# Kernel tuning notes

Hardware: AMD Instinct MI355X
Metric: run time of the kernel (lower is better)

The kernel has to match this reference:

```python
import jax, jax.numpy as jnp
import numpy as np

N_NODES = 50000
N_EDGES = 800000


def setup_inputs() -> dict:
    key = jax.random.key(0)
    ks = jax.random.split(key, 6)
    x = jax.random.normal(ks[0], (N_NODES, 22), dtype=jnp.float32)
    # small weight scale to keep tanh in its linear-ish regime
    W0 = jax.random.normal(ks[1], (22, 220), dtype=jnp.float32) * 0.1
    W1 = jax.random.normal(ks[2], (220, 220), dtype=jnp.float32) * 0.05
    W2 = jax.random.normal(ks[3], (220, 220), dtype=jnp.float32) * 0.05
    W3 = jax.random.normal(ks[4], (220, 10), dtype=jnp.float32) * 0.05
    b0 = jnp.zeros((220,), jnp.float32)
    b1 = jnp.zeros((220,), jnp.float32)
    b2 = jnp.zeros((220,), jnp.float32)
    b3 = jnp.zeros((10,), jnp.float32)
    edge_index = jax.random.randint(ks[5], (2, N_EDGES), 0, N_NODES, dtype=jnp.int64)
    return {"x": x, "W0": W0, "b0": b0, "W1": W1, "b1": b1,
            "W2": W2, "b2": b2, "W3": W3, "b3": b3, "edge_index": edge_index}


def _graph_conv(h, W, b, src, dst, inv_sqrt_out, inv_sqrt_in, activation):
    # DGL GraphConv, norm='both':
    #   h' = D_in^{-1/2} * A^T * (D_out^{-1/2} * h) @ W + b
    h = h * inv_sqrt_out[:, None]          # [N, F_in]
    m = h[src]                             # gather: [E, F_in]
    agg = jax.ops.segment_sum(m, dst, num_segments=N_NODES)  # scatter-add: [N, F_in]
    agg = agg * inv_sqrt_in[:, None]
    out = agg @ W + b
    if activation is not None:
        out = activation(out)
    return out


def reference(x, W0, b0, W1, b1, W2, b2, W3, b3, edge_index):
    src, dst = edge_index[0], edge_index[1]
    ones = jnp.ones((edge_index.shape[1],), jnp.float32)
    deg_out = jax.ops.segment_sum(ones, src, num_segments=N_NODES)
    deg_in = jax.ops.segment_sum(ones, dst, num_segments=N_NODES)
    inv_sqrt_out = jax.lax.rsqrt(jnp.maximum(deg_out, 1.0))
    inv_sqrt_in = jax.lax.rsqrt(jnp.maximum(deg_in, 1.0))

    h = _graph_conv(x, W0, b0, src, dst, inv_sqrt_out, inv_sqrt_in, jnp.tanh)
    h = _graph_conv(h, W1, b1, src, dst, inv_sqrt_out, inv_sqrt_in, jnp.tanh)
    h = _graph_conv(h, W2, b2, src, dst, inv_sqrt_out, inv_sqrt_in, jnp.tanh)
    h = _graph_conv(h, W3, b3, src, dst, inv_sqrt_out, inv_sqrt_in, None)
    return h
```

## Files before the change

kernel.cpp:

```cpp
#include <hip/hip_runtime.h>
#include <math.h>

#define N_NODES 50000
#define N_EDGES 800000
#define NPAD 50176
#define HSTR 224

typedef __attribute__((ext_vector_type(8))) short short8;
typedef __attribute__((ext_vector_type(4))) float f32x4;
typedef __attribute__((ext_vector_type(4))) _Float16 half4;


__device__ __forceinline__ float fast_tanh(float x) {
    float e = __expf(2.0f * x);
    float r = __builtin_amdgcn_rcpf(e + 1.0f);
    return 1.0f - 2.0f * r;
}

__device__ __forceinline__ unsigned short rne_bf16(float x) {
    unsigned u = __builtin_bit_cast(unsigned, x);
    return (unsigned short)((u + 0x7FFFu + ((u >> 16) & 1u)) >> 16);
}

__device__ __forceinline__ void split_bf16(float x, unsigned short& hi, unsigned short& lo) {
    hi = rne_bf16(x);
    float hf = __builtin_bit_cast(float, (unsigned)hi << 16);
    lo = rne_bf16(x - hf);
}

__device__ __forceinline__ f32x4 mfma16(short8 a, short8 b, f32x4 c) {
    return __builtin_amdgcn_mfma_f32_16x16x32_bf16(a, b, c, 0, 0, 0);
}

__device__ __forceinline__ void wsplit_one(const float* __restrict__ W, int KIN, int LDA,
                                           unsigned short* __restrict__ WT_hi,
                                           unsigned short* __restrict__ WT_lo, int idx) {
    int n = idx / LDA;
    int k = idx - n * LDA;
    float v = (n < 220 && k < KIN) ? W[k * 220 + n] : 0.f;
    unsigned short hi, lo;
    split_bf16(v, hi, lo);
    WT_hi[idx] = hi;
    WT_lo[idx] = lo;
}


__global__ void k_hist_wsplit(const int* __restrict__ ei, int* __restrict__ deg_out,
                              int* __restrict__ ecsbuf, int* __restrict__ rank,
                              const float* __restrict__ W0, const float* __restrict__ W1,
                              const float* __restrict__ W2,
                              unsigned short* __restrict__ wt0h, unsigned short* __restrict__ wt0l,
                              unsigned short* __restrict__ wt1h, unsigned short* __restrict__ wt1l,
                              unsigned short* __restrict__ wt2h, unsigned short* __restrict__ wt2l) {
    int bx = blockIdx.x;
    if (bx < 3125) {
        int e = bx * 256 + threadIdx.x;
        if (e < N_EDGES) {
            atomicAdd(&deg_out[ei[e]], 1);
            rank[e] = atomicAdd(&ecsbuf[1 + ei[N_EDGES + e]], 1);
        }
    } else if (bx < 3153) {
        int idx = (bx - 3125) * 256 + threadIdx.x;
        if (idx < 224 * 32) wsplit_one(W0, 22, 32, wt0h, wt0l, idx);
    } else if (bx < 3349) {
        int idx = (bx - 3153) * 256 + threadIdx.x;
        wsplit_one(W1, 220, 224, wt1h, wt1l, idx);
    } else {
        int idx = (bx - 3349) * 256 + threadIdx.x;
        wsplit_one(W2, 220, 224, wt2h, wt2l, idx);
    }
}

__global__ void k_scan1(const int* __restrict__ in, int* __restrict__ out,
                        int* __restrict__ bsum, int n) {
    __shared__ int s[256];
    int i = blockIdx.x * 256 + threadIdx.x;
    int v = (i < n) ? in[i] : 0;
    s[threadIdx.x] = v;
    __syncthreads();
    for (int off = 1; off < 256; off <<= 1) {
        int t = (threadIdx.x >= off) ? s[threadIdx.x - off] : 0;
        __syncthreads();
        s[threadIdx.x] += t;
        __syncthreads();
    }
    if (i < n) out[i] = s[threadIdx.x] - v;
    if (threadIdx.x == 255 && bsum) bsum[blockIdx.x] = s[255];
}

__global__ void k_scan_mid(int* __restrict__ a, int n) {
    __shared__ int s[256];
    __shared__ int carry;
    if (threadIdx.x == 0) carry = 0;
    for (int base = 0; base < n; base += 256) {
        int i = base + threadIdx.x;
        int v = (i < n) ? a[i] : 0;
        s[threadIdx.x] = v;
        __syncthreads();
        for (int off = 1; off < 256; off <<= 1) {
            int t = (threadIdx.x >= off) ? s[threadIdx.x - off] : 0;
            __syncthreads();
            s[threadIdx.x] += t;
            __syncthreads();
        }
        int c = carry;
        if (i < n) a[i] = s[threadIdx.x] - v + c;
        __syncthreads();
        if (threadIdx.x == 0) carry = c + s[255];
        __syncthreads();
    }
}

__global__ void k_scan3(int* __restrict__ out, const int* __restrict__ bscan, int n) {
    int i = blockIdx.x * 256 + threadIdx.x;
    if (i < n) out[i] += bscan[blockIdx.x];
}

__global__ void k_post_scan(const int* __restrict__ ei, const int* __restrict__ ecsbuf,
                            const int* __restrict__ rank, const int* __restrict__ deg_out,
                            const float* __restrict__ x,
                            float* __restrict__ inv_out, float* __restrict__ inv_in,
                            int* __restrict__ src_sorted, float* __restrict__ xs) {
    int bx = blockIdx.x;
    if (bx < 196) {
        int n = bx * 256 + threadIdx.x;
        if (n >= N_NODES) return;
        int di = ecsbuf[n + 2] - ecsbuf[n + 1];
        int a = deg_out[n]; if (a < 1) a = 1;
        if (di < 1) di = 1;
        inv_out[n] = 1.0f / sqrtf((float)a);
        inv_in[n]  = 1.0f / sqrtf((float)di);
    } else if (bx < 3321) {
        int e = (bx - 196) * 256 + threadIdx.x;
        if (e < N_EDGES) {
            int d = ei[N_EDGES + e];
            src_sorted[ecsbuf[1 + d] + rank[e]] = ei[e];
        }
    } else {
        int idx = (bx - 3321) * 256 + threadIdx.x;
        if (idx >= N_NODES * 11) return;
        int n = idx / 11;
        int f2 = idx - n * 11;
        int a = deg_out[n]; if (a < 1) a = 1;
        float sc = 1.0f / sqrtf((float)a);
        float2 v = *(const float2*)&x[n * 22 + f2 * 2];
        v.x *= sc; v.y *= sc;
        *(float2*)&xs[n * 22 + f2 * 2] = v;
    }
}


__global__ void k_agg22_split(const float* __restrict__ xs,
                              const int* __restrict__ ecsbuf, const int* __restrict__ srcs,
                              const float* __restrict__ inv_in,
                              unsigned short* __restrict__ A_hi, unsigned short* __restrict__ A_lo) {
    int idx = blockIdx.x * 256 + threadIdx.x;
    int n = idx >> 4, f2 = idx & 15;
    if (n >= N_NODES) return;
    float ax = 0.f, ay = 0.f;
    if (f2 <= 10) {
        const float2* xb = (const float2*)(xs) + f2;
        int e = ecsbuf[n + 1], end = ecsbuf[n + 2];
        for (; e + 3 < end; e += 4) {
            int s0 = srcs[e], s1 = srcs[e + 1], s2 = srcs[e + 2], s3 = srcs[e + 3];
            float2 v0 = xb[s0 * 11], v1 = xb[s1 * 11];
            float2 v2 = xb[s2 * 11], v3 = xb[s3 * 11];
            ax += (v0.x + v1.x) + (v2.x + v3.x);
            ay += (v0.y + v1.y) + (v2.y + v3.y);
        }
        for (; e < end; ++e) {
            float2 v0 = xb[srcs[e] * 11];
            ax += v0.x;
            ay += v0.y;
        }
        float si = inv_in[n];
        ax *= si; ay *= si;
    }
    ushort2 h2, l2;
    split_bf16(ax, h2.x, l2.x);
    split_bf16(ay, h2.y, l2.y);
    *(ushort2*)&A_hi[n * 32 + f2 * 2] = h2;
    *(ushort2*)&A_lo[n * 32 + f2 * 2] = l2;
}

__global__ __launch_bounds__(256) void k_agg220_split(const _Float16* __restrict__ h,
                                                      const int* __restrict__ ecsbuf,
                                                      const int* __restrict__ srcs,
                                                      const float* __restrict__ inv_in,
                                                      unsigned short* __restrict__ A_hi,
                                                      unsigned short* __restrict__ A_lo) {
    int lane = threadIdx.x & 63;
    int n = blockIdx.x * 4 + (threadIdx.x >> 6);
    if (n >= N_NODES || lane >= 56) return;
    size_t ob = (size_t)n * 224 + lane * 4;
    if (lane == 55) {
        ushort4 z = {0, 0, 0, 0};
        *(ushort4*)&A_hi[ob] = z;
        *(ushort4*)&A_lo[ob] = z;
        return;
    }
    int f4 = lane * 4;
    const _Float16* hb = h + f4;
    int e = ecsbuf[n + 1], end = ecsbuf[n + 2];
    float4 a0 = {0,0,0,0}, a1 = {0,0,0,0}, a2 = {0,0,0,0}, a3 = {0,0,0,0};
    for (; e + 7 < end; e += 8) {
        int s0 = srcs[e],     s1 = srcs[e + 1], s2 = srcs[e + 2], s3 = srcs[e + 3];
        int s4 = srcs[e + 4], s5 = srcs[e + 5], s6 = srcs[e + 6], s7 = srcs[e + 7];
        half4 v0 = *(const half4*)(hb + (size_t)s0 * HSTR);
        half4 v1 = *(const half4*)(hb + (size_t)s1 * HSTR);
        half4 v2 = *(const half4*)(hb + (size_t)s2 * HSTR);
        half4 v3 = *(const half4*)(hb + (size_t)s3 * HSTR);
        half4 v4 = *(const half4*)(hb + (size_t)s4 * HSTR);
        half4 v5 = *(const half4*)(hb + (size_t)s5 * HSTR);
        half4 v6 = *(const half4*)(hb + (size_t)s6 * HSTR);
        half4 v7 = *(const half4*)(hb + (size_t)s7 * HSTR);
        a0.x += (float)v0.x; a0.y += (float)v0.y; a0.z += (float)v0.z; a0.w += (float)v0.w;
        a1.x += (float)v1.x; a1.y += (float)v1.y; a1.z += (float)v1.z; a1.w += (float)v1.w;
        a2.x += (float)v2.x; a2.y += (float)v2.y; a2.z += (float)v2.z; a2.w += (float)v2.w;
        a3.x += (float)v3.x; a3.y += (float)v3.y; a3.z += (float)v3.z; a3.w += (float)v3.w;
        a0.x += (float)v4.x; a0.y += (float)v4.y; a0.z += (float)v4.z; a0.w += (float)v4.w;
        a1.x += (float)v5.x; a1.y += (float)v5.y; a1.z += (float)v5.z; a1.w += (float)v5.w;
        a2.x += (float)v6.x; a2.y += (float)v6.y; a2.z += (float)v6.z; a2.w += (float)v6.w;
        a3.x += (float)v7.x; a3.y += (float)v7.y; a3.z += (float)v7.z; a3.w += (float)v7.w;
    }
    for (; e + 3 < end; e += 4) {
        int s0 = srcs[e], s1 = srcs[e + 1], s2 = srcs[e + 2], s3 = srcs[e + 3];
        half4 v0 = *(const half4*)(hb + (size_t)s0 * HSTR);
        half4 v1 = *(const half4*)(hb + (size_t)s1 * HSTR);
        half4 v2 = *(const half4*)(hb + (size_t)s2 * HSTR);
        half4 v3 = *(const half4*)(hb + (size_t)s3 * HSTR);
        a0.x += (float)v0.x; a0.y += (float)v0.y; a0.z += (float)v0.z; a0.w += (float)v0.w;
        a1.x += (float)v1.x; a1.y += (float)v1.y; a1.z += (float)v1.z; a1.w += (float)v1.w;
        a2.x += (float)v2.x; a2.y += (float)v2.y; a2.z += (float)v2.z; a2.w += (float)v2.w;
        a3.x += (float)v3.x; a3.y += (float)v3.y; a3.z += (float)v3.z; a3.w += (float)v3.w;
    }
    for (; e < end; ++e) {
        half4 v = *(const half4*)(hb + (size_t)srcs[e] * HSTR);
        a0.x += (float)v.x; a0.y += (float)v.y; a0.z += (float)v.z; a0.w += (float)v.w;
    }
    float sc = inv_in[n];
    float4 t;
    t.x = ((a0.x + a1.x) + (a2.x + a3.x)) * sc;
    t.y = ((a0.y + a1.y) + (a2.y + a3.y)) * sc;
    t.z = ((a0.z + a1.z) + (a2.z + a3.z)) * sc;
    t.w = ((a0.w + a1.w) + (a2.w + a3.w)) * sc;
    ushort4 h4, l4;
    split_bf16(t.x, h4.x, l4.x);
    split_bf16(t.y, h4.y, l4.y);
    split_bf16(t.z, h4.z, l4.z);
    split_bf16(t.w, h4.w, l4.w);
    *(ushort4*)&A_hi[ob] = h4;
    *(ushort4*)&A_lo[ob] = l4;
}

__global__ void k_agg10_epi(const float* __restrict__ tmp, const int* __restrict__ ecsbuf,
                            const int* __restrict__ srcs, const float* __restrict__ inv_in,
                            const float* __restrict__ bias, float* __restrict__ out) {
    int idx = blockIdx.x * 256 + threadIdx.x;
    if (idx >= N_NODES * 5) return;
    int n = idx / 5;
    int f2 = idx - n * 5;
    const float2* tb0 = (const float2*)(tmp) + f2;
    const float2* tb1 = (const float2*)(tmp + (size_t)NPAD * 10) + f2;
    float ax = 0.f, ay = 0.f;
    int e = ecsbuf[n + 1], end = ecsbuf[n + 2];
    for (; e + 1 < end; e += 2) {
        float2 u0 = tb0[srcs[e] * 5],     w0 = tb1[srcs[e] * 5];
        float2 u1 = tb0[srcs[e + 1] * 5], w1 = tb1[srcs[e + 1] * 5];
        ax += (u0.x + w0.x) + (u1.x + w1.x);
        ay += (u0.y + w0.y) + (u1.y + w1.y);
    }
    if (e < end) {
        float2 u0 = tb0[srcs[e] * 5], w0 = tb1[srcs[e] * 5];
        ax += u0.x + w0.x;
        ay += u0.y + w0.y;
    }
    float si = inv_in[n];
    float2 o;
    o.x = ax * si + bias[f2 * 2];
    o.y = ay * si + bias[f2 * 2 + 1];
    *(float2*)&out[n * 10 + f2 * 2] = o;
}

template <int KSTEPS, int LDA, bool FUSE_W3>
__global__ __launch_bounds__(256, 4) void k_gemm_mfma(const unsigned short* __restrict__ A_hi,
                                                      const unsigned short* __restrict__ A_lo,
                                                      const unsigned short* __restrict__ WT_hi,
                                                      const unsigned short* __restrict__ WT_lo,
                                                      const float* __restrict__ bias,
                                                      const float* __restrict__ post,
                                                      _Float16* __restrict__ out,
                                                      const float* __restrict__ W3,
                                                      float* __restrict__ tmp) {
    int tid = threadIdx.x;
    int l = tid & 63, w = tid >> 6;
    int lrow = l & 15, q = l >> 4;
    int bid = blockIdx.x;
    int ch = bid & 1;
    int rt = (bid >> 1) * 64 + w * 16;
    int cb = ch * 112;

    const unsigned short* pah = A_hi + (size_t)(rt + lrow) * LDA + q * 8;
    const unsigned short* pal = A_lo + (size_t)(rt + lrow) * LDA + q * 8;
    const unsigned short* pbh = WT_hi + (size_t)(cb + lrow) * LDA + q * 8;
    const unsigned short* pbl = WT_lo + (size_t)(cb + lrow) * LDA + q * 8;

    f32x4 acc[7];
#pragma unroll
    for (int ct = 0; ct < 7; ++ct) acc[ct] = (f32x4){0.f, 0.f, 0.f, 0.f};

#pragma unroll
    for (int ks = 0; ks < KSTEPS; ++ks) {
        int k0 = ks * 32;
        short8 ah = *(const short8*)(const void*)(pah + k0);
        short8 al = *(const short8*)(const void*)(pal + k0);
#pragma unroll
        for (int ct = 0; ct < 7; ++ct) {
            size_t boff = (size_t)(ct * 16) * LDA + k0;
            short8 bh = *(const short8*)(const void*)(pbh + boff);
            short8 bl = *(const short8*)(const void*)(pbl + boff);
            acc[ct] = mfma16(ah, bh, acc[ct]);
            acc[ct] = mfma16(ah, bl, acc[ct]);
            acc[ct] = mfma16(al, bh, acc[ct]);
        }
    }

    float pv[4];
#pragma unroll
    for (int r = 0; r < 4; ++r) {
        int r0 = rt + q * 4 + r;
        pv[r] = (r0 < N_NODES) ? post[r0] : 0.f;
    }

    if (!FUSE_W3) {
#pragma unroll
        for (int ct = 0; ct < 7; ++ct) {
            int col = cb + ct * 16 + lrow;
            if (col >= 220) continue;
            float bv = bias[col];
#pragma unroll
            for (int r = 0; r < 4; ++r) {
                int r0 = rt + q * 4 + r;
                if (r0 < N_NODES)
                    out[(size_t)r0 * HSTR + col] = (_Float16)(pv[r] * fast_tanh(acc[ct][r] + bv));
            }
        }
    } else {
        float p[4][10];
#pragma unroll
        for (int r = 0; r < 4; ++r)
#pragma unroll
            for (int j = 0; j < 10; ++j) p[r][j] = 0.f;
#pragma unroll
        for (int ct = 0; ct < 7; ++ct) {
            int col = cb + ct * 16 + lrow;
            bool cok = col < 220;
            float bv = cok ? bias[col] : 0.f;
            float w3v[10];
            if (cok) {
                const float2* wp = (const float2*)&W3[col * 10];
#pragma unroll
                for (int j2 = 0; j2 < 5; ++j2) {
                    float2 t = wp[j2];
                    w3v[2 * j2] = t.x;
                    w3v[2 * j2 + 1] = t.y;
                }
            } else {
#pragma unroll
                for (int j = 0; j < 10; ++j) w3v[j] = 0.f;
            }
#pragma unroll
            for (int r = 0; r < 4; ++r) {
                float h2 = pv[r] * fast_tanh(acc[ct][r] + bv);
#pragma unroll
                for (int j = 0; j < 10; ++j) p[r][j] += h2 * w3v[j];
            }
        }
#pragma unroll
        for (int r = 0; r < 4; ++r)
#pragma unroll
            for (int j = 0; j < 10; ++j) {
                float v = p[r][j];
                v += __shfl_xor(v, 1, 64);
                v += __shfl_xor(v, 2, 64);
                v += __shfl_xor(v, 4, 64);
                v += __shfl_xor(v, 8, 64);
                p[r][j] = v;
            }
        if (lrow == 0) {
#pragma unroll
            for (int r = 0; r < 4; ++r) {
                int row = rt + q * 4 + r;
                if (row < N_NODES) {
                    float* tp = tmp + ((size_t)ch * NPAD + row) * 10;
#pragma unroll
                    for (int j2 = 0; j2 < 5; ++j2) {
                        float2 o = {p[r][2 * j2], p[r][2 * j2 + 1]};
                        *(float2*)&tp[2 * j2] = o;
                    }
                }
            }
        }
    }
}


extern "C" void kernel_launch(void* const* d_in, const int* in_sizes, int n_in,
                              void* d_out, int out_size, void* d_ws, size_t ws_size,
                              hipStream_t stream) {
    const float* x  = (const float*)d_in[0];
    const float* W0 = (const float*)d_in[1];
    const float* b0 = (const float*)d_in[2];
    const float* W1 = (const float*)d_in[3];
    const float* b1 = (const float*)d_in[4];
    const float* W2 = (const float*)d_in[5];
    const float* b2 = (const float*)d_in[6];
    const float* W3 = (const float*)d_in[7];
    const float* b3 = (const float*)d_in[8];
    const int*   ei = (const int*)d_in[9];
    float* out = (float*)d_out;

    int* ws = (int*)d_ws;
    int* ecsbuf     = ws + 0;
    int* deg_out    = ws + 50432;
    int* bsumA      = ws + 100608;
    float* inv_out  = (float*)(ws + 100864);
    float* inv_in   = (float*)(ws + 151040);
    int* src_sorted = ws + 201216;
    unsigned short* wt0h = (unsigned short*)(ws + 1001216);
    unsigned short* wt0l = (unsigned short*)(ws + 1004800);
    unsigned short* wt1h = (unsigned short*)(ws + 1008384);
    unsigned short* wt1l = (unsigned short*)(ws + 1033472);
    unsigned short* wt2h = (unsigned short*)(ws + 1058560);
    unsigned short* wt2l = (unsigned short*)(ws + 1083648);
    unsigned short* ahi  = (unsigned short*)(ws + 1108736);
    unsigned short* alo  = (unsigned short*)(ws + 6728448);
    _Float16* hbuf = (_Float16*)(ws + 12348160);
    float* tmp10 = (float*)(ws + 17948160);
    int* rank    = (int*)ahi;
    float* xs    = (float*)(ws + 1108736 + 3000000);

    hipMemsetAsync(ws, 0, (size_t)100608 * sizeof(int), stream);

    k_hist_wsplit<<<3545, 256, 0, stream>>>(ei, deg_out, ecsbuf, rank,
                                            W0, W1, W2, wt0h, wt0l, wt1h, wt1l, wt2h, wt2l);
    k_scan1<<<196, 256, 0, stream>>>(ecsbuf + 1, ecsbuf + 1, bsumA, NPAD);
    k_scan_mid<<<1, 256, 0, stream>>>(bsumA, 196);
    k_scan3<<<196, 256, 0, stream>>>(ecsbuf + 1, bsumA, NPAD);
    k_post_scan<<<5470, 256, 0, stream>>>(ei, ecsbuf, rank, deg_out, x,
                                          inv_out, inv_in, src_sorted, xs);

    int gemm_grid = (NPAD / 64) * 2;
    int agg_grid  = (N_NODES + 3) / 4;

    k_agg22_split<<<(N_NODES * 16 + 255) / 256, 256, 0, stream>>>(
        xs, ecsbuf, src_sorted, inv_in, ahi, alo);
    k_gemm_mfma<1, 32, false><<<gemm_grid, 256, 0, stream>>>(
        ahi, alo, wt0h, wt0l, b0, inv_out, hbuf, nullptr, nullptr);

    k_agg220_split<<<agg_grid, 256, 0, stream>>>(hbuf, ecsbuf, src_sorted, inv_in, ahi, alo);
    k_gemm_mfma<7, 224, false><<<gemm_grid, 256, 0, stream>>>(
        ahi, alo, wt1h, wt1l, b1, inv_out, hbuf, nullptr, nullptr);

    k_agg220_split<<<agg_grid, 256, 0, stream>>>(hbuf, ecsbuf, src_sorted, inv_in, ahi, alo);
    k_gemm_mfma<7, 224, true><<<gemm_grid, 256, 0, stream>>>(
        ahi, alo, wt2h, wt2l, b2, inv_out, nullptr, W3, tmp10);

    k_agg10_epi<<<(N_NODES * 5 + 255) / 256, 256, 0, stream>>>(
        tmp10, ecsbuf, src_sorted, inv_in, b3, out);
}
```

Baseline: 465.8 us.

## Double rows per warp in MFMA GEMM and batch histogram edges per thread

Each warp in the split-bf16 MFMA GEMM now computes two 16-row tiles instead of one, so every B (weight) fragment loaded is reused across twice as many rows. Block row coverage goes from 64 to 128 and the grid is halved. The launch-bounds occupancy hint drops from 4 to 3 to make room for the doubled accumulators. Separately, the histogram kernel has each thread handle four edges, cutting its block count; the cost is higher register pressure and fewer waves for latency hiding.

Result: no change. 473.8 us (+1.7%).

```diff
diff --git a/kernel.cpp b/kernel.cpp
--- a/kernel.cpp
+++ b/kernel.cpp
@@ -53,20 +53,24 @@
                               unsigned short* __restrict__ wt1h, unsigned short* __restrict__ wt1l,
                               unsigned short* __restrict__ wt2h, unsigned short* __restrict__ wt2l) {
     int bx = blockIdx.x;
-    if (bx < 3125) {
-        int e = bx * 256 + threadIdx.x;
-        if (e < N_EDGES) {
-            atomicAdd(&deg_out[ei[e]], 1);
-            rank[e] = atomicAdd(&ecsbuf[1 + ei[N_EDGES + e]], 1);
-        }
-    } else if (bx < 3153) {
-        int idx = (bx - 3125) * 256 + threadIdx.x;
+    if (bx < 782) {
+        int base = bx * 1024 + threadIdx.x;
+#pragma unroll
+        for (int i = 0; i < 4; ++i) {
+            int e = base + i * 256;
+            if (e < N_EDGES) {
+                atomicAdd(&deg_out[ei[e]], 1);
+                rank[e] = atomicAdd(&ecsbuf[1 + ei[N_EDGES + e]], 1);
+            }
+        }
+    } else if (bx < 810) {
+        int idx = (bx - 782) * 256 + threadIdx.x;
         if (idx < 224 * 32) wsplit_one(W0, 22, 32, wt0h, wt0l, idx);
-    } else if (bx < 3349) {
-        int idx = (bx - 3153) * 256 + threadIdx.x;
+    } else if (bx < 1006) {
+        int idx = (bx - 810) * 256 + threadIdx.x;
         wsplit_one(W1, 220, 224, wt1h, wt1l, idx);
     } else {
-        int idx = (bx - 3349) * 256 + threadIdx.x;
+        int idx = (bx - 1006) * 256 + threadIdx.x;
         wsplit_one(W2, 220, 224, wt2h, wt2l, idx);
     }
 }
@@ -283,7 +287,7 @@
 }
 
 template <int KSTEPS, int LDA, bool FUSE_W3>
-__global__ __launch_bounds__(256, 4) void k_gemm_mfma(const unsigned short* __restrict__ A_hi,
+__global__ __launch_bounds__(256, 3) void k_gemm_mfma(const unsigned short* __restrict__ A_hi,
                                                       const unsigned short* __restrict__ A_lo,
                                                       const unsigned short* __restrict__ WT_hi,
                                                       const unsigned short* __restrict__ WT_lo,
@@ -297,39 +301,51 @@
     int lrow = l & 15, q = l >> 4;
     int bid = blockIdx.x;
     int ch = bid & 1;
-    int rt = (bid >> 1) * 64 + w * 16;
+    int rt = (bid >> 1) * 128 + w * 32;
     int cb = ch * 112;
 
-    const unsigned short* pah = A_hi + (size_t)(rt + lrow) * LDA + q * 8;
-    const unsigned short* pal = A_lo + (size_t)(rt + lrow) * LDA + q * 8;
+    const unsigned short* pa0h = A_hi + (size_t)(rt + lrow) * LDA + q * 8;
+    const unsigned short* pa0l = A_lo + (size_t)(rt + lrow) * LDA + q * 8;
+    const unsigned short* pa1h = pa0h + 16 * LDA;
+    const unsigned short* pa1l = pa0l + 16 * LDA;
     const unsigned short* pbh = WT_hi + (size_t)(cb + lrow) * LDA + q * 8;
     const unsigned short* pbl = WT_lo + (size_t)(cb + lrow) * LDA + q * 8;
 
-    f32x4 acc[7];
-#pragma unroll
-    for (int ct = 0; ct < 7; ++ct) acc[ct] = (f32x4){0.f, 0.f, 0.f, 0.f};
+    f32x4 acc0[7], acc1[7];
+#pragma unroll
+    for (int ct = 0; ct < 7; ++ct) {
+        acc0[ct] = (f32x4){0.f, 0.f, 0.f, 0.f};
+        acc1[ct] = (f32x4){0.f, 0.f, 0.f, 0.f};
+    }
 
 #pragma unroll
     for (int ks = 0; ks < KSTEPS; ++ks) {
         int k0 = ks * 32;
-        short8 ah = *(const short8*)(const void*)(pah + k0);
-        short8 al = *(const short8*)(const void*)(pal + k0);
+        short8 ah0 = *(const short8*)(const void*)(pa0h + k0);
+        short8 al0 = *(const short8*)(const void*)(pa0l + k0);
+        short8 ah1 = *(const short8*)(const void*)(pa1h + k0);
+        short8 al1 = *(const short8*)(const void*)(pa1l + k0);
 #pragma unroll
         for (int ct = 0; ct < 7; ++ct) {
             size_t boff = (size_t)(ct * 16) * LDA + k0;
             short8 bh = *(const short8*)(const void*)(pbh + boff);
             short8 bl = *(const short8*)(const void*)(pbl + boff);
-            acc[ct] = mfma16(ah, bh, acc[ct]);
-            acc[ct] = mfma16(ah, bl, acc[ct]);
-            acc[ct] = mfma16(al, bh, acc[ct]);
-        }
-    }
-
-    float pv[4];
+            acc0[ct] = mfma16(ah0, bh, acc0[ct]);
+            acc0[ct] = mfma16(ah0, bl, acc0[ct]);
+            acc0[ct] = mfma16(al0, bh, acc0[ct]);
+            acc1[ct] = mfma16(ah1, bh, acc1[ct]);
+            acc1[ct] = mfma16(ah1, bl, acc1[ct]);
+            acc1[ct] = mfma16(al1, bh, acc1[ct]);
+        }
+    }
+
+    float pv0[4], pv1[4];
 #pragma unroll
     for (int r = 0; r < 4; ++r) {
         int r0 = rt + q * 4 + r;
-        pv[r] = (r0 < N_NODES) ? post[r0] : 0.f;
+        int r1 = r0 + 16;
+        pv0[r] = (r0 < N_NODES) ? post[r0] : 0.f;
+        pv1[r] = (r1 < N_NODES) ? post[r1] : 0.f;
     }
 
     if (!FUSE_W3) {
@@ -341,62 +357,71 @@
 #pragma unroll
             for (int r = 0; r < 4; ++r) {
                 int r0 = rt + q * 4 + r;
+                int r1 = r0 + 16;
                 if (r0 < N_NODES)
-                    out[(size_t)r0 * HSTR + col] = (_Float16)(pv[r] * fast_tanh(acc[ct][r] + bv));
+                    out[(size_t)r0 * HSTR + col] = (_Float16)(pv0[r] * fast_tanh(acc0[ct][r] + bv));
+                if (r1 < N_NODES)
+                    out[(size_t)r1 * HSTR + col] = (_Float16)(pv1[r] * fast_tanh(acc1[ct][r] + bv));
             }
         }
     } else {
-        float p[4][10];
-#pragma unroll
-        for (int r = 0; r < 4; ++r)
-#pragma unroll
-            for (int j = 0; j < 10; ++j) p[r][j] = 0.f;
-#pragma unroll
-        for (int ct = 0; ct < 7; ++ct) {
-            int col = cb + ct * 16 + lrow;
-            bool cok = col < 220;
-            float bv = cok ? bias[col] : 0.f;
-            float w3v[10];
-            if (cok) {
-                const float2* wp = (const float2*)&W3[col * 10];
-#pragma unroll
-                for (int j2 = 0; j2 < 5; ++j2) {
-                    float2 t = wp[j2];
-                    w3v[2 * j2] = t.x;
-                    w3v[2 * j2 + 1] = t.y;
+#pragma unroll
+        for (int half = 0; half < 2; ++half) {
+            const f32x4* acc = half ? acc1 : acc0;
+            const float* pv  = half ? pv1 : pv0;
+            int rbase = rt + half * 16;
+            float p[4][10];
+#pragma unroll
+            for (int r = 0; r < 4; ++r)
+#pragma unroll
+                for (int j = 0; j < 10; ++j) p[r][j] = 0.f;
+#pragma unroll
+            for (int ct = 0; ct < 7; ++ct) {
+                int col = cb + ct * 16 + lrow;
+                bool cok = col < 220;
+                float bv = cok ? bias[col] : 0.f;
+                float w3v[10];
+                if (cok) {
+                    const float2* wp = (const float2*)&W3[col * 10];
+#pragma unroll
+                    for (int j2 = 0; j2 < 5; ++j2) {
+                        float2 t = wp[j2];
+                        w3v[2 * j2] = t.x;
+                        w3v[2 * j2 + 1] = t.y;
+                    }
+                } else {
+#pragma unroll
+                    for (int j = 0; j < 10; ++j) w3v[j] = 0.f;
                 }
-            } else {
-#pragma unroll
-                for (int j = 0; j < 10; ++j) w3v[j] = 0.f;
+#pragma unroll
+                for (int r = 0; r < 4; ++r) {
+                    float h2 = pv[r] * fast_tanh(acc[ct][r] + bv);
+#pragma unroll
+                    for (int j = 0; j < 10; ++j) p[r][j] += h2 * w3v[j];
+                }
             }
 #pragma unroll
-            for (int r = 0; r < 4; ++r) {
-                float h2 = pv[r] * fast_tanh(acc[ct][r] + bv);
-#pragma unroll
-                for (int j = 0; j < 10; ++j) p[r][j] += h2 * w3v[j];
-            }
-        }
-#pragma unroll
-        for (int r = 0; r < 4; ++r)
-#pragma unroll
-            for (int j = 0; j < 10; ++j) {
-                float v = p[r][j];
-                v += __shfl_xor(v, 1, 64);
-                v += __shfl_xor(v, 2, 64);
-                v += __shfl_xor(v, 4, 64);
-                v += __shfl_xor(v, 8, 64);
-                p[r][j] = v;
-            }
-        if (lrow == 0) {
-#pragma unroll
-            for (int r = 0; r < 4; ++r) {
-                int row = rt + q * 4 + r;
-                if (row < N_NODES) {
-                    float* tp = tmp + ((size_t)ch * NPAD + row) * 10;
-#pragma unroll
-                    for (int j2 = 0; j2 < 5; ++j2) {
-                        float2 o = {p[r][2 * j2], p[r][2 * j2 + 1]};
-                        *(float2*)&tp[2 * j2] = o;
+            for (int r = 0; r < 4; ++r)
+#pragma unroll
+                for (int j = 0; j < 10; ++j) {
+                    float v = p[r][j];
+                    v += __shfl_xor(v, 1, 64);
+                    v += __shfl_xor(v, 2, 64);
+                    v += __shfl_xor(v, 4, 64);
+                    v += __shfl_xor(v, 8, 64);
+                    p[r][j] = v;
+                }
+            if (lrow == 0) {
+#pragma unroll
+                for (int r = 0; r < 4; ++r) {
+                    int row = rbase + q * 4 + r;
+                    if (row < N_NODES) {
+                        float* tp = tmp + ((size_t)ch * NPAD + row) * 10;
+#pragma unroll
+                        for (int j2 = 0; j2 < 5; ++j2) {
+                            float2 o = {p[r][2 * j2], p[r][2 * j2 + 1]};
+                            *(float2*)&tp[2 * j2] = o;
+                        }
                     }
                 }
             }
@@ -442,7 +467,7 @@
 
     hipMemsetAsync(ws, 0, (size_t)100608 * sizeof(int), stream);
 
-    k_hist_wsplit<<<3545, 256, 0, stream>>>(ei, deg_out, ecsbuf, rank,
+    k_hist_wsplit<<<1202, 256, 0, stream>>>(ei, deg_out, ecsbuf, rank,
                                             W0, W1, W2, wt0h, wt0l, wt1h, wt1l, wt2h, wt2l);
     k_scan1<<<196, 256, 0, stream>>>(ecsbuf + 1, ecsbuf + 1, bsumA, NPAD);
     k_scan_mid<<<1, 256, 0, stream>>>(bsumA, 196);
@@ -450,7 +475,7 @@
     k_post_scan<<<5470, 256, 0, stream>>>(ei, ecsbuf, rank, deg_out, x,
                                           inv_out, inv_in, src_sorted, xs);
 
-    int gemm_grid = (NPAD / 64) * 2;
+    int gemm_grid = (NPAD / 128) * 2;
     int agg_grid  = (N_NODES + 3) / 4;
 
     k_agg22_split<<<(N_NODES * 16 + 255) / 256, 256, 0, stream>>>(
```

## Compute full 224 columns per GEMM block and drop partial-sum split in layer 3

Applied to the files above, without the earlier changes.

The MFMA GEMM now has each wave compute all 14 column tiles instead of splitting columns across two blocks. This halves the grid and removes the redundant A-fragment reloads. In the W3-fused layer, the two half-column partial outputs and their summation in the final aggregation are no longer needed, so k_agg10_epi gathers one buffer instead of two. The histogram kernel also processes four edges per thread with fewer blocks. The cost is twice as many accumulator registers under launch_bounds(256,4), which risks spills or lower occupancy, and half as many blocks to spread across the GPU.

Result: slower. 577.9 us (+24.1%).

```diff
diff --git a/kernel.cpp b/kernel.cpp
--- a/kernel.cpp
+++ b/kernel.cpp
@@ -53,20 +53,24 @@
                               unsigned short* __restrict__ wt1h, unsigned short* __restrict__ wt1l,
                               unsigned short* __restrict__ wt2h, unsigned short* __restrict__ wt2l) {
     int bx = blockIdx.x;
-    if (bx < 3125) {
-        int e = bx * 256 + threadIdx.x;
-        if (e < N_EDGES) {
-            atomicAdd(&deg_out[ei[e]], 1);
-            rank[e] = atomicAdd(&ecsbuf[1 + ei[N_EDGES + e]], 1);
-        }
-    } else if (bx < 3153) {
-        int idx = (bx - 3125) * 256 + threadIdx.x;
+    if (bx < 782) {
+        int base = bx * 1024 + threadIdx.x;
+#pragma unroll
+        for (int i = 0; i < 4; ++i) {
+            int e = base + i * 256;
+            if (e < N_EDGES) {
+                atomicAdd(&deg_out[ei[e]], 1);
+                rank[e] = atomicAdd(&ecsbuf[1 + ei[N_EDGES + e]], 1);
+            }
+        }
+    } else if (bx < 810) {
+        int idx = (bx - 782) * 256 + threadIdx.x;
         if (idx < 224 * 32) wsplit_one(W0, 22, 32, wt0h, wt0l, idx);
-    } else if (bx < 3349) {
-        int idx = (bx - 3153) * 256 + threadIdx.x;
+    } else if (bx < 1006) {
+        int idx = (bx - 810) * 256 + threadIdx.x;
         wsplit_one(W1, 220, 224, wt1h, wt1l, idx);
     } else {
-        int idx = (bx - 3349) * 256 + threadIdx.x;
+        int idx = (bx - 1006) * 256 + threadIdx.x;
         wsplit_one(W2, 220, 224, wt2h, wt2l, idx);
     }
 }
@@ -260,20 +264,19 @@
     if (idx >= N_NODES * 5) return;
     int n = idx / 5;
     int f2 = idx - n * 5;
-    const float2* tb0 = (const float2*)(tmp) + f2;
-    const float2* tb1 = (const float2*)(tmp + (size_t)NPAD * 10) + f2;
+    const float2* tb = (const float2*)(tmp) + f2;
     float ax = 0.f, ay = 0.f;
     int e = ecsbuf[n + 1], end = ecsbuf[n + 2];
     for (; e + 1 < end; e += 2) {
-        float2 u0 = tb0[srcs[e] * 5],     w0 = tb1[srcs[e] * 5];
-        float2 u1 = tb0[srcs[e + 1] * 5], w1 = tb1[srcs[e + 1] * 5];
-        ax += (u0.x + w0.x) + (u1.x + w1.x);
-        ay += (u0.y + w0.y) + (u1.y + w1.y);
+        float2 v0 = tb[srcs[e] * 5];
+        float2 v1 = tb[srcs[e + 1] * 5];
+        ax += v0.x + v1.x;
+        ay += v0.y + v1.y;
     }
     if (e < end) {
-        float2 u0 = tb0[srcs[e] * 5], w0 = tb1[srcs[e] * 5];
-        ax += u0.x + w0.x;
-        ay += u0.y + w0.y;
+        float2 v0 = tb[srcs[e] * 5];
+        ax += v0.x;
+        ay += v0.y;
     }
     float si = inv_in[n];
     float2 o;
@@ -295,19 +298,16 @@
     int tid = threadIdx.x;
     int l = tid & 63, w = tid >> 6;
     int lrow = l & 15, q = l >> 4;
-    int bid = blockIdx.x;
-    int ch = bid & 1;
-    int rt = (bid >> 1) * 64 + w * 16;
-    int cb = ch * 112;
+    int rt = blockIdx.x * 64 + w * 16;
 
     const unsigned short* pah = A_hi + (size_t)(rt + lrow) * LDA + q * 8;
     const unsigned short* pal = A_lo + (size_t)(rt + lrow) * LDA + q * 8;
-    const unsigned short* pbh = WT_hi + (size_t)(cb + lrow) * LDA + q * 8;
-    const unsigned short* pbl = WT_lo + (size_t)(cb + lrow) * LDA + q * 8;
-
-    f32x4 acc[7];
-#pragma unroll
-    for (int ct = 0; ct < 7; ++ct) acc[ct] = (f32x4){0.f, 0.f, 0.f, 0.f};
+    const unsigned short* pbh = WT_hi + (size_t)lrow * LDA + q * 8;
+    const unsigned short* pbl = WT_lo + (size_t)lrow * LDA + q * 8;
+
+    f32x4 acc[14];
+#pragma unroll
+    for (int ct = 0; ct < 14; ++ct) acc[ct] = (f32x4){0.f, 0.f, 0.f, 0.f};
 
 #pragma unroll
     for (int ks = 0; ks < KSTEPS; ++ks) {
@@ -315,7 +315,7 @@
         short8 ah = *(const short8*)(const void*)(pah + k0);
         short8 al = *(const short8*)(const void*)(pal + k0);
 #pragma unroll
-        for (int ct = 0; ct < 7; ++ct) {
+        for (int ct = 0; ct < 14; ++ct) {
             size_t boff = (size_t)(ct * 16) * LDA + k0;
             short8 bh = *(const short8*)(const void*)(pbh + boff);
             short8 bl = *(const short8*)(const void*)(pbl + boff);
@@ -334,8 +334,8 @@
 
     if (!FUSE_W3) {
 #pragma unroll
-        for (int ct = 0; ct < 7; ++ct) {
-            int col = cb + ct * 16 + lrow;
+        for (int ct = 0; ct < 14; ++ct) {
+            int col = ct * 16 + lrow;
             if (col >= 220) continue;
             float bv = bias[col];
 #pragma unroll
@@ -346,57 +346,60 @@
             }
         }
     } else {
-        float p[4][10];
-#pragma unroll
-        for (int r = 0; r < 4; ++r)
-#pragma unroll
-            for (int j = 0; j < 10; ++j) p[r][j] = 0.f;
-#pragma unroll
-        for (int ct = 0; ct < 7; ++ct) {
-            int col = cb + ct * 16 + lrow;
-            bool cok = col < 220;
-            float bv = cok ? bias[col] : 0.f;
-            float w3v[10];
-            if (cok) {
-                const float2* wp = (const float2*)&W3[col * 10];
-#pragma unroll
-                for (int j2 = 0; j2 < 5; ++j2) {
-                    float2 t = wp[j2];
-                    w3v[2 * j2] = t.x;
-                    w3v[2 * j2 + 1] = t.y;
+#pragma unroll
+        for (int rc = 0; rc < 2; ++rc) {
+            float p[2][10];
+#pragma unroll
+            for (int r2 = 0; r2 < 2; ++r2)
+#pragma unroll
+                for (int j = 0; j < 10; ++j) p[r2][j] = 0.f;
+#pragma unroll
+            for (int ct = 0; ct < 14; ++ct) {
+                int col = ct * 16 + lrow;
+                bool cok = col < 220;
+                float bv = cok ? bias[col] : 0.f;
+                float w3v[10];
+                if (cok) {
+                    const float2* wp = (const float2*)&W3[col * 10];
+#pragma unroll
+                    for (int j2 = 0; j2 < 5; ++j2) {
+                        float2 t = wp[j2];
+                        w3v[2 * j2] = t.x;
+                        w3v[2 * j2 + 1] = t.y;
+                    }
+                } else {
+#pragma unroll
+                    for (int j = 0; j < 10; ++j) w3v[j] = 0.f;
                 }
-            } else {
-#pragma unroll
-                for (int j = 0; j < 10; ++j) w3v[j] = 0.f;
+#pragma unroll
+                for (int r2 = 0; r2 < 2; ++r2) {
+                    int r = rc * 2 + r2;
+                    float h2 = pv[r] * fast_tanh(acc[ct][r] + bv);
+#pragma unroll
+                    for (int j = 0; j < 10; ++j) p[r2][j] += h2 * w3v[j];
+                }
             }
 #pragma unroll
-            for (int r = 0; r < 4; ++r) {
-                float h2 = pv[r] * fast_tanh(acc[ct][r] + bv);
-#pragma unroll
-                for (int j = 0; j < 10; ++j) p[r][j] += h2 * w3v[j];
-            }
-        }
-#pragma unroll
-        for (int r = 0; r < 4; ++r)
-#pragma unroll
-            for (int j = 0; j < 10; ++j) {
-                float v = p[r][j];
-                v += __shfl_xor(v, 1, 64);
-                v += __shfl_xor(v, 2, 64);
-                v += __shfl_xor(v, 4, 64);
-                v += __shfl_xor(v, 8, 64);
-                p[r][j] = v;
-            }
-        if (lrow == 0) {
-#pragma unroll
-            for (int r = 0; r < 4; ++r) {
-                int row = rt + q * 4 + r;
-                if (row < N_NODES) {
-                    float* tp = tmp + ((size_t)ch * NPAD + row) * 10;
-#pragma unroll
-                    for (int j2 = 0; j2 < 5; ++j2) {
-                        float2 o = {p[r][2 * j2], p[r][2 * j2 + 1]};
-                        *(float2*)&tp[2 * j2] = o;
+            for (int r2 = 0; r2 < 2; ++r2)
+#pragma unroll
+                for (int j = 0; j < 10; ++j) {
+                    float v = p[r2][j];
+                    v += __shfl_xor(v, 1, 64);
+                    v += __shfl_xor(v, 2, 64);
+                    v += __shfl_xor(v, 4, 64);
+                    v += __shfl_xor(v, 8, 64);
+                    p[r2][j] = v;
+                }
+            if (lrow == 0) {
+#pragma unroll
+                for (int r2 = 0; r2 < 2; ++r2) {
+                    int row = rt + q * 4 + rc * 2 + r2;
+                    if (row < N_NODES) {
+#pragma unroll
+                        for (int j2 = 0; j2 < 5; ++j2) {
+                            float2 o = {p[r2][2 * j2], p[r2][2 * j2 + 1]};
+                            *(float2*)&tmp[(size_t)row * 10 + 2 * j2] = o;
+                        }
                     }
                 }
             }
@@ -442,7 +445,7 @@
 
     hipMemsetAsync(ws, 0, (size_t)100608 * sizeof(int), stream);
 
-    k_hist_wsplit<<<3545, 256, 0, stream>>>(ei, deg_out, ecsbuf, rank,
+    k_hist_wsplit<<<1202, 256, 0, stream>>>(ei, deg_out, ecsbuf, rank,
                                             W0, W1, W2, wt0h, wt0l, wt1h, wt1l, wt2h, wt2l);
     k_scan1<<<196, 256, 0, stream>>>(ecsbuf + 1, ecsbuf + 1, bsumA, NPAD);
     k_scan_mid<<<1, 256, 0, stream>>>(bsumA, 196);
@@ -450,7 +453,7 @@
     k_post_scan<<<5470, 256, 0, stream>>>(ei, ecsbuf, rank, deg_out, x,
                                           inv_out, inv_in, src_sorted, xs);
 
-    int gemm_grid = (NPAD / 64) * 2;
+    int gemm_grid = NPAD / 64;
     int agg_grid  = (N_NODES + 3) / 4;
 
     k_agg22_split<<<(N_NODES * 16 + 255) / 256, 256, 0, stream>>>(
```

## Privatize degree histograms into eight copies to cut atomic contention

Applied to the files above, without the earlier changes.

The degree/count histogram is split into eight private copies chosen by block index, each block now handles four edges per thread, and the rank is packed together with the copy id. A new k_sum8 kernel reduces the copies into per-copy prefix offsets and totals, and the scatter into sorted order adds the per-copy prefix. This is meant to spread same-address atomics over eight locations. In exchange it adds a kernel launch and a larger memset, and the pass keeps its existing cost on 800K edges.

After: 466.2 us. About the same (+0.1%).

```diff
diff --git a/kernel.cpp b/kernel.cpp
--- a/kernel.cpp
+++ b/kernel.cpp
@@ -45,30 +45,57 @@
 }
 
 
-__global__ void k_hist_wsplit(const int* __restrict__ ei, int* __restrict__ deg_out,
-                              int* __restrict__ ecsbuf, int* __restrict__ rank,
+__global__ void k_hist_wsplit(const int* __restrict__ ei, int* __restrict__ deg8,
+                              int* __restrict__ cnt8, int* __restrict__ rank,
                               const float* __restrict__ W0, const float* __restrict__ W1,
                               const float* __restrict__ W2,
                               unsigned short* __restrict__ wt0h, unsigned short* __restrict__ wt0l,
                               unsigned short* __restrict__ wt1h, unsigned short* __restrict__ wt1l,
                               unsigned short* __restrict__ wt2h, unsigned short* __restrict__ wt2l) {
     int bx = blockIdx.x;
-    if (bx < 3125) {
-        int e = bx * 256 + threadIdx.x;
-        if (e < N_EDGES) {
-            atomicAdd(&deg_out[ei[e]], 1);
-            rank[e] = atomicAdd(&ecsbuf[1 + ei[N_EDGES + e]], 1);
-        }
-    } else if (bx < 3153) {
-        int idx = (bx - 3125) * 256 + threadIdx.x;
+    if (bx < 782) {
+        int c = bx & 7;
+        int* degc = deg8 + c * NPAD;
+        int* cntc = cnt8 + c * NPAD;
+        int base = bx * 1024 + threadIdx.x;
+#pragma unroll
+        for (int i = 0; i < 4; ++i) {
+            int e = base + i * 256;
+            if (e < N_EDGES) {
+                atomicAdd(&degc[ei[e]], 1);
+                int r = atomicAdd(&cntc[ei[N_EDGES + e]], 1);
+                rank[e] = (r << 3) | c;
+            }
+        }
+    } else if (bx < 810) {
+        int idx = (bx - 782) * 256 + threadIdx.x;
         if (idx < 224 * 32) wsplit_one(W0, 22, 32, wt0h, wt0l, idx);
-    } else if (bx < 3349) {
-        int idx = (bx - 3153) * 256 + threadIdx.x;
+    } else if (bx < 1006) {
+        int idx = (bx - 810) * 256 + threadIdx.x;
         wsplit_one(W1, 220, 224, wt1h, wt1l, idx);
     } else {
-        int idx = (bx - 3349) * 256 + threadIdx.x;
+        int idx = (bx - 1006) * 256 + threadIdx.x;
         wsplit_one(W2, 220, 224, wt2h, wt2l, idx);
     }
+}
+
+__global__ void k_sum8(int* __restrict__ cnt8, const int* __restrict__ deg8,
+                       int* __restrict__ ecsbuf, int* __restrict__ deg_out) {
+    int d = blockIdx.x * 256 + threadIdx.x;
+    if (d >= NPAD) return;
+    int s = 0;
+#pragma unroll
+    for (int c = 0; c < 8; ++c) {
+        int v = cnt8[c * NPAD + d];
+        cnt8[c * NPAD + d] = s;
+        s += v;
+    }
+    ecsbuf[1 + d] = s;
+    if (d == 0) ecsbuf[0] = 0;
+    int t = 0;
+#pragma unroll
+    for (int c = 0; c < 8; ++c) t += deg8[c * NPAD + d];
+    deg_out[d] = t;
 }
 
 __global__ void k_scan1(const int* __restrict__ in, int* __restrict__ out,
@@ -117,8 +144,8 @@
 }
 
 __global__ void k_post_scan(const int* __restrict__ ei, const int* __restrict__ ecsbuf,
-                            const int* __restrict__ rank, const int* __restrict__ deg_out,
-                            const float* __restrict__ x,
+                            const int* __restrict__ rank, const int* __restrict__ prefix8,
+                            const int* __restrict__ deg_out, const float* __restrict__ x,
                             float* __restrict__ inv_out, float* __restrict__ inv_in,
                             int* __restrict__ src_sorted, float* __restrict__ xs) {
     int bx = blockIdx.x;
@@ -134,7 +161,9 @@
         int e = (bx - 196) * 256 + threadIdx.x;
         if (e < N_EDGES) {
             int d = ei[N_EDGES + e];
-            src_sorted[ecsbuf[1 + d] + rank[e]] = ei[e];
+            int rc = rank[e];
+            int c = rc & 7, r = rc >> 3;
+            src_sorted[ecsbuf[1 + d] + prefix8[c * NPAD + d] + r] = ei[e];
         }
     } else {
         int idx = (bx - 3321) * 256 + threadIdx.x;
@@ -437,17 +466,20 @@
     unsigned short* alo  = (unsigned short*)(ws + 6728448);
     _Float16* hbuf = (_Float16*)(ws + 12348160);
     float* tmp10 = (float*)(ws + 17948160);
-    int* rank    = (int*)ahi;
-    float* xs    = (float*)(ws + 1108736 + 3000000);
-
-    hipMemsetAsync(ws, 0, (size_t)100608 * sizeof(int), stream);
-
-    k_hist_wsplit<<<3545, 256, 0, stream>>>(ei, deg_out, ecsbuf, rank,
+    int* rank  = (int*)ahi;
+    int* cnt8  = (int*)alo;
+    int* deg8  = (int*)alo + 8 * NPAD;
+    float* xs  = (float*)(ws + 1108736 + 3000000);
+
+    hipMemsetAsync(cnt8, 0, (size_t)16 * NPAD * sizeof(int), stream);
+
+    k_hist_wsplit<<<1202, 256, 0, stream>>>(ei, deg8, cnt8, rank,
                                             W0, W1, W2, wt0h, wt0l, wt1h, wt1l, wt2h, wt2l);
+    k_sum8<<<196, 256, 0, stream>>>(cnt8, deg8, ecsbuf, deg_out);
     k_scan1<<<196, 256, 0, stream>>>(ecsbuf + 1, ecsbuf + 1, bsumA, NPAD);
     k_scan_mid<<<1, 256, 0, stream>>>(bsumA, 196);
     k_scan3<<<196, 256, 0, stream>>>(ecsbuf + 1, bsumA, NPAD);
-    k_post_scan<<<5470, 256, 0, stream>>>(ei, ecsbuf, rank, deg_out, x,
+    k_post_scan<<<5470, 256, 0, stream>>>(ei, ecsbuf, rank, cnt8, deg_out, x,
                                           inv_out, inv_in, src_sorted, xs);
 
     int gemm_grid = (NPAD / 64) * 2;
```
